# Kernel tuning notes

Measured on AMD Instinct MI355X. Metric: run time of the kernel, lower is better.

The kernel has to match this reference:

```python
import jax, jax.numpy as jnp
import numpy as np
from jax import lax

D_MODEL, D_STATE, D_CONV, EXPAND = 512, 16, 4, 2
D_INNER = EXPAND * D_MODEL          # 1024
DT_RANK = (D_MODEL + 15) // 16      # 32
BATCH, SEQ = 4, 1024


def setup_inputs() -> dict:
    key = jax.random.key(0)
    ks = jax.random.split(key, 8)
    s = 0.02
    x = jax.random.normal(ks[0], (BATCH, SEQ, D_MODEL), jnp.float32)
    in_proj_w = jax.random.normal(ks[1], (2 * D_INNER, D_MODEL), jnp.float32) * s
    conv_w = jax.random.normal(ks[2], (D_INNER, 1, D_CONV), jnp.float32) * s  # depthwise
    conv_b = jnp.zeros((D_INNER,), jnp.float32)
    x_proj_w = jax.random.normal(ks[3], (DT_RANK + 2 * D_STATE, D_INNER), jnp.float32) * s
    dt_proj_w = jax.random.normal(ks[4], (D_INNER, DT_RANK), jnp.float32) * s
    dt_proj_b = jax.random.normal(ks[5], (D_INNER,), jnp.float32) * 0.1
    # Mamba S4D-real init: A = -[1..d_state] per channel, stored as log
    A_log = jnp.log(jnp.tile(jnp.arange(1, D_STATE + 1, dtype=jnp.float32)[None, :], (D_INNER, 1)))
    D = jnp.ones((D_INNER,), jnp.float32)
    out_proj_w = jax.random.normal(ks[6], (D_MODEL, D_INNER), jnp.float32) * s
    ln_w = jnp.ones((D_MODEL,), jnp.float32)
    ln_b = jnp.zeros((D_MODEL,), jnp.float32)
    return dict(x=x, in_proj_w=in_proj_w, conv_w=conv_w, conv_b=conv_b,
                x_proj_w=x_proj_w, dt_proj_w=dt_proj_w, dt_proj_b=dt_proj_b,
                A_log=A_log, D=D, out_proj_w=out_proj_w, ln_w=ln_w, ln_b=ln_b)


def _selective_scan(u, delta, A, Bm, Cm, D):
    # u, delta: (B,L,Di); A: (Di,N); Bm, Cm: (B,L,N)
    dA = jnp.exp(delta[..., None] * A)                    # (B,L,Di,N)
    dBu = (delta * u)[..., None] * Bm[:, :, None, :]      # (B,L,Di,N)
    dA_t = jnp.moveaxis(dA, 1, 0)                         # (L,B,Di,N)
    dBu_t = jnp.moveaxis(dBu, 1, 0)
    C_t = jnp.moveaxis(Cm, 1, 0)                          # (L,B,N)

    def step(h, inp):
        dA_i, dBu_i, C_i = inp
        h = dA_i * h + dBu_i                              # (B,Di,N)
        y = jnp.einsum('bdn,bn->bd', h, C_i)
        return h, y

    h0 = jnp.zeros((u.shape[0], A.shape[0], A.shape[1]), u.dtype)
    _, ys = lax.scan(step, h0, (dA_t, dBu_t, C_t))        # ys: (L,B,Di)
    return jnp.moveaxis(ys, 0, 1) + u * D                 # (B,L,Di)


def reference(x, in_proj_w, conv_w, conv_b, x_proj_w, dt_proj_w, dt_proj_b,
              A_log, D, out_proj_w, ln_w, ln_b):
    # ---- Mamba SSM ----
    xz = jnp.einsum('bld,ed->ble', x, in_proj_w)          # (B,L,2*Di)
    xs, z = jnp.split(xz, 2, axis=-1)
    # causal depthwise conv over time
    xt = jnp.moveaxis(xs, 1, 2)                           # (B,Di,L)
    xt = lax.conv_general_dilated(xt, conv_w, window_strides=(1,),
                                  padding=[(D_CONV - 1, 0)],
                                  feature_group_count=D_INNER,
                                  dimension_numbers=('NCH', 'OIH', 'NCH'))
    xt = xt + conv_b[None, :, None]
    u = jax.nn.silu(jnp.moveaxis(xt, 1, 2))               # (B,L,Di)

    x_dbl = jnp.einsum('bld,ed->ble', u, x_proj_w)        # (B,L,dt_rank+2N)
    dt = x_dbl[..., :DT_RANK]
    Bm = x_dbl[..., DT_RANK:DT_RANK + D_STATE]
    Cm = x_dbl[..., DT_RANK + D_STATE:]
    delta = jax.nn.softplus(jnp.einsum('blr,dr->bld', dt, dt_proj_w) + dt_proj_b)
    A = -jnp.exp(A_log)                                   # (Di,N)

    y = _selective_scan(u, delta, A, Bm, Cm, D)
    y = y * jax.nn.silu(z)
    ssm_out = jnp.einsum('ble,de->bld', y, out_proj_w)    # (B,L,Dm)

    # ---- residual + LayerNorm ----
    r = x + ssm_out
    mu = jnp.mean(r, axis=-1, keepdims=True)
    var = jnp.mean(jnp.square(r - mu), axis=-1, keepdims=True)
    return (r - mu) / jnp.sqrt(var + 1e-5) * ln_w + ln_b
```

## Files before the change

kernel.cpp:

```cpp
#include <hip/hip_runtime.h>
#include <hip/hip_bf16.h>
#include <math.h>

#define B_   4
#define L_   1024
#define DM   512
#define DI   1024
#define NS   16
#define XDC  64
#define BL   4096
#define G_   16
#define SEG  64
#define KS   4

typedef short bfrag __attribute__((ext_vector_type(8)));
typedef float ffrag __attribute__((ext_vector_type(4)));

__device__ __forceinline__ ushort f2bf(float v) {
    __hip_bfloat16 h = __float2bfloat16(v);
    return *(ushort*)&h;
}

__global__ __launch_bounds__(256) void cast_bf16(const float* __restrict__ in,
        ushort* __restrict__ out, int n4)
{
    int i = blockIdx.x * 256 + threadIdx.x;
    if (i >= n4) return;
    float4 v = ((const float4*)in)[i];
    ushort4 o;
    o.x = f2bf(v.x); o.y = f2bf(v.y); o.z = f2bf(v.z); o.w = f2bf(v.w);
    ((ushort4*)out)[i] = o;
}

template<int EPI>
__global__ __launch_bounds__(256) void gemm_mfma(const ushort* __restrict__ A,
        const ushort* __restrict__ B, float* __restrict__ C,
        int K, int ldc, const float* __restrict__ resid,
        const float* __restrict__ bias)
{
    __shared__ ushort As[128][40];
    __shared__ ushort Bs[128][40];
    const int tid = threadIdx.x;
    const int lane = tid & 63, wave = tid >> 6;
    const int wm = (wave & 1) * 64, wn = (wave >> 1) * 64;
    const int l15 = lane & 15, quad = lane >> 4;
    const int m0 = blockIdx.y * 128, n0 = blockIdx.x * 128;

    ffrag acc[4][4] = {};

    for (int k0 = 0; k0 < K; k0 += 32) {
        #pragma unroll
        for (int i = 0; i < 2; i++) {
            int chunk = tid + i * 256;
            int row = chunk >> 2, kk8 = (chunk & 3) * 8;
            *(uint4*)&As[row][kk8] = *(const uint4*)&A[(size_t)(m0 + row) * K + k0 + kk8];
            *(uint4*)&Bs[row][kk8] = *(const uint4*)&B[(size_t)(n0 + row) * K + k0 + kk8];
        }
        __syncthreads();
        bfrag af[4], bfv[4];
        #pragma unroll
        for (int i = 0; i < 4; i++) {
            af[i]  = *(const bfrag*)&As[wm + i * 16 + l15][quad * 8];
            bfv[i] = *(const bfrag*)&Bs[wn + i * 16 + l15][quad * 8];
        }
        #pragma unroll
        for (int i = 0; i < 4; i++)
            #pragma unroll
            for (int j = 0; j < 4; j++)
                acc[i][j] = __builtin_amdgcn_mfma_f32_16x16x32_bf16(af[i], bfv[j], acc[i][j], 0, 0, 0);
        __syncthreads();
    }

    #pragma unroll
    for (int i = 0; i < 4; i++) {
        #pragma unroll
        for (int j = 0; j < 4; j++) {
            int n = n0 + wn + j * 16 + l15;
            #pragma unroll
            for (int r = 0; r < 4; r++) {
                int m = m0 + wm + i * 16 + quad * 4 + r;
                float v = acc[i][j][r];
                if (EPI == 2) v += resid[(size_t)m * ldc + n];
                if (EPI == 3) {
                    v += bias[m];
                    v = (v > 20.f) ? v : log1pf(__expf(v));
                }
                C[(size_t)m * ldc + n] = v;
            }
        }
    }
}

__global__ __launch_bounds__(256) void gemm3_splitk(const float* __restrict__ uT,
        const float* __restrict__ xw, float* __restrict__ part)
{
    __shared__ float As[16][33];
    __shared__ float Ws[16][68];
    const int tid = threadIdx.x;
    const int tx = tid & 15, ty = tid >> 4;
    const int ks = blockIdx.x, m0 = blockIdx.y * 32;
    const int kbase = ks * (DI / KS);
    float acc[2][4] = {};

    for (int k0 = 0; k0 < DI / KS; k0 += 16) {
        if (tid < 128) {
            int k = tid >> 3, m4 = (tid & 7) * 4;
            const float4 v = *(const float4*)&uT[(size_t)(kbase + k0 + k) * BL + m0 + m4];
            As[k][m4 + 0] = v.x; As[k][m4 + 1] = v.y;
            As[k][m4 + 2] = v.z; As[k][m4 + 3] = v.w;
        }
        {
            int r = tid >> 2, c4 = (tid & 3) * 4;
            const float4 v = *(const float4*)&xw[(size_t)r * DI + kbase + k0 + c4];
            Ws[c4 + 0][r] = v.x; Ws[c4 + 1][r] = v.y;
            Ws[c4 + 2][r] = v.z; Ws[c4 + 3][r] = v.w;
        }
        __syncthreads();
        #pragma unroll
        for (int kk = 0; kk < 16; kk++) {
            float a[2], b[4];
            a[0] = As[kk][ty * 2 + 0];
            a[1] = As[kk][ty * 2 + 1];
            #pragma unroll
            for (int j = 0; j < 4; j++) b[j] = Ws[kk][tx * 4 + j];
            #pragma unroll
            for (int i = 0; i < 2; i++)
                #pragma unroll
                for (int j = 0; j < 4; j++)
                    acc[i][j] = fmaf(a[i], b[j], acc[i][j]);
        }
        __syncthreads();
    }

    float* pp = part + (size_t)ks * BL * XDC;
    #pragma unroll
    for (int i = 0; i < 2; i++) {
        int m = m0 + ty * 2 + i;
        *(float4*)&pp[(size_t)m * XDC + tx * 4] =
            make_float4(acc[i][0], acc[i][1], acc[i][2], acc[i][3]);
    }
}

__global__ __launch_bounds__(256) void gemm3_reduce(const float* __restrict__ part,
        float* __restrict__ xdbl, ushort* __restrict__ dtB)
{
    int i = blockIdx.x * 256 + threadIdx.x;
    const float4* p0 = (const float4*)part;
    float4 a = p0[i];
    #pragma unroll
    for (int s = 1; s < KS; s++) {
        float4 b = p0[i + (size_t)s * BL * XDC / 4];
        a.x += b.x; a.y += b.y; a.z += b.z; a.w += b.w;
    }
    ((float4*)xdbl)[i] = a;
    int c4 = i & 15;
    if (c4 < 8) {
        int m = i >> 4;
        ushort4 o;
        o.x = f2bf(a.x); o.y = f2bf(a.y); o.z = f2bf(a.z); o.w = f2bf(a.w);
        ((ushort4*)dtB)[m * 8 + c4] = o;
    }
}

__global__ __launch_bounds__(256) void conv_silu(const float* __restrict__ xzT,
        const float* __restrict__ cw, const float* __restrict__ cb,
        float* __restrict__ uT)
{
    int i = blockIdx.x * 256 + threadIdx.x;
    int d  = i >> 10;
    int q  = i & 1023;
    int bl = q * 4;
    int l  = bl & (L_ - 1);
    const float* row = xzT + (size_t)d * BL;
    float4 cur = *(const float4*)&row[bl];
    float4 prev = make_float4(0.f, 0.f, 0.f, 0.f);
    if (l != 0) prev = *(const float4*)&row[bl - 4];
    float v[7] = { prev.y, prev.z, prev.w, cur.x, cur.y, cur.z, cur.w };
    float w0 = cw[d * 4 + 0], w1 = cw[d * 4 + 1], w2 = cw[d * 4 + 2], w3 = cw[d * 4 + 3];
    float bias = cb[d];
    float4 o;
    o.x = bias + w0 * v[0] + w1 * v[1] + w2 * v[2] + w3 * v[3];
    o.y = bias + w0 * v[1] + w1 * v[2] + w2 * v[3] + w3 * v[4];
    o.z = bias + w0 * v[2] + w1 * v[3] + w2 * v[4] + w3 * v[5];
    o.w = bias + w0 * v[3] + w1 * v[4] + w2 * v[5] + w3 * v[6];
    o.x = o.x / (1.f + __expf(-o.x));
    o.y = o.y / (1.f + __expf(-o.y));
    o.z = o.z / (1.f + __expf(-o.z));
    o.w = o.w / (1.f + __expf(-o.w));
    *(float4*)&uT[(size_t)d * BL + bl] = o;
}

__global__ __launch_bounds__(256) void scan_fused(const float* __restrict__ deltaT,
        const float* __restrict__ uT, const float* __restrict__ xdbl,
        const float* __restrict__ xzT, const float* __restrict__ A_log,
        const float* __restrict__ Dp, float* __restrict__ yT)
{
    __shared__ float hend_s[G_][NS + 1];
    __shared__ float h0_s[G_][NS + 1];
    __shared__ float sdv_s[G_];

    const int tid = threadIdx.x;
    const int n = tid & 15;
    const int seg = tid >> 4;
    const int bd = blockIdx.x;
    const int d = bd & (DI - 1);
    const int b = bd >> 10;

    const float Acoef = -__expf(A_log[d * NS + n]);
    const float Dd = Dp[d];

    const size_t base_t = (size_t)d * BL + b * L_ + seg * SEG;
    const size_t base_z = (size_t)(DI + d) * BL + b * L_ + seg * SEG;
    const size_t base_x = (size_t)b * L_ * XDC + (size_t)seg * SEG * XDC;

    float h = 0.f, sdv = 0.f;
    for (int l0 = 0; l0 < SEG; l0 += 16) {
        float dv[16], uv[16], Bv[16];
        {
            const float4* dp = (const float4*)(deltaT + base_t + l0);
            const float4* up = (const float4*)(uT + base_t + l0);
            #pragma unroll
            for (int i = 0; i < 4; i++) {
                *(float4*)&dv[i * 4] = dp[i];
                *(float4*)&uv[i * 4] = up[i];
            }
        }
        {
            const float* xp = xdbl + base_x + (size_t)l0 * XDC + 32 + n;
            #pragma unroll
            for (int j = 0; j < 16; j++) Bv[j] = xp[j * XDC];
        }
        #pragma unroll
        for (int j = 0; j < 16; j++) {
            sdv += dv[j];
            Bv[j] *= dv[j] * uv[j];
            dv[j] = __expf(dv[j] * Acoef);
        }
        #pragma unroll
        for (int j = 0; j < 16; j++)
            h = fmaf(dv[j], h, Bv[j]);
    }
    hend_s[seg][n] = h;
    if (n == 0) sdv_s[seg] = sdv;
    __syncthreads();

    if (seg == 0) {
        float H = 0.f;
        #pragma unroll
        for (int s = 0; s < G_; s++) {
            h0_s[s][n] = H;
            H = hend_s[s][n] + __expf(Acoef * sdv_s[s]) * H;
        }
    }
    __syncthreads();

    h = h0_s[seg][n];
    for (int l0 = 0; l0 < SEG; l0 += 16) {
        float ug = uT [base_t + l0 + n];
        float zg = xzT[base_z + l0 + n];

        float dv[16], uv[16];
        {
            const float4* dp = (const float4*)(deltaT + base_t + l0);
            const float4* up = (const float4*)(uT + base_t + l0);
            #pragma unroll
            for (int i = 0; i < 4; i++) {
                *(float4*)&dv[i * 4] = dp[i];
                *(float4*)&uv[i * 4] = up[i];
            }
        }
        float Bv[16], Cv[16];
        {
            const float* xp = xdbl + base_x + (size_t)l0 * XDC + 32 + n;
            #pragma unroll
            for (int j = 0; j < 16; j++) {
                Bv[j] = xp[j * XDC];
                Cv[j] = xp[j * XDC + 16];
            }
        }
        #pragma unroll
        for (int j = 0; j < 16; j++) {
            Bv[j] *= dv[j] * uv[j];
            dv[j] = __expf(dv[j] * Acoef);
        }
        float p[16];
        #pragma unroll
        for (int j = 0; j < 16; j++) {
            h = fmaf(dv[j], h, Bv[j]);
            p[j] = h * Cv[j];
        }

        float q8[8];
        #pragma unroll
        for (int k = 0; k < 8; k++) {
            float tt = (n & 8) ? p[k] : p[k + 8];
            float rr = __shfl_xor(tt, 8);
            q8[k] = ((n & 8) ? p[k + 8] : p[k]) + rr;
        }
        float q4[4];
        #pragma unroll
        for (int k = 0; k < 4; k++) {
            float tt = (n & 4) ? q8[k] : q8[k + 4];
            float rr = __shfl_xor(tt, 4);
            q4[k] = ((n & 4) ? q8[k + 4] : q8[k]) + rr;
        }
        float q2[2];
        #pragma unroll
        for (int k = 0; k < 2; k++) {
            float tt = (n & 2) ? q4[k] : q4[k + 2];
            float rr = __shfl_xor(tt, 2);
            q2[k] = ((n & 2) ? q4[k + 2] : q4[k]) + rr;
        }
        float tt = (n & 1) ? q2[0] : q2[1];
        float rr = __shfl_xor(tt, 1);
        float S = ((n & 1) ? q2[1] : q2[0]) + rr;

        float v = S + ug * Dd;
        v *= zg / (1.f + __expf(-zg));
        yT[base_t + l0 + n] = v;
    }
}

__global__ __launch_bounds__(256) void transpose_cast(const float* __restrict__ yT,
        ushort* __restrict__ yB)
{
    __shared__ float t[64][65];
    const int bl0 = blockIdx.x * 64, d0 = blockIdx.y * 64;
    const int tid = threadIdx.x;
    #pragma unroll
    for (int i = 0; i < 4; i++) {
        int chunk = tid + i * 256;
        int dr = chunk >> 4, c4 = (chunk & 15) * 4;
        const float4 v = *(const float4*)&yT[(size_t)(d0 + dr) * BL + bl0 + c4];
        t[dr][c4 + 0] = v.x; t[dr][c4 + 1] = v.y;
        t[dr][c4 + 2] = v.z; t[dr][c4 + 3] = v.w;
    }
    __syncthreads();
    #pragma unroll
    for (int i = 0; i < 4; i++) {
        int chunk = tid + i * 256;
        int br = chunk >> 4, dc4 = (chunk & 15) * 4;
        ushort4 o;
        o.x = f2bf(t[dc4 + 0][br]); o.y = f2bf(t[dc4 + 1][br]);
        o.z = f2bf(t[dc4 + 2][br]); o.w = f2bf(t[dc4 + 3][br]);
        *(ushort4*)&yB[(size_t)(bl0 + br) * DI + d0 + dc4] = o;
    }
}

__global__ __launch_bounds__(256) void ln_kernel(const float* __restrict__ r,
        const float* __restrict__ lnw, const float* __restrict__ lnb,
        float* __restrict__ out)
{
    int row = blockIdx.x;
    const float* rr = r + (size_t)row * DM;
    float v0 = rr[threadIdx.x], v1 = rr[threadIdx.x + 256];
    float s = v0 + v1, s2 = v0 * v0 + v1 * v1;
    #pragma unroll
    for (int off = 32; off > 0; off >>= 1) {
        s  += __shfl_down(s, off);
        s2 += __shfl_down(s2, off);
    }
    __shared__ float ls[4], ls2[4];
    __shared__ float mu_s, rstd_s;
    int wid = threadIdx.x >> 6, lane = threadIdx.x & 63;
    if (lane == 0) { ls[wid] = s; ls2[wid] = s2; }
    __syncthreads();
    if (threadIdx.x == 0) {
        float S = ls[0] + ls[1] + ls[2] + ls[3];
        float S2 = ls2[0] + ls2[1] + ls2[2] + ls2[3];
        float mu = S * (1.f / DM);
        float var = S2 * (1.f / DM) - mu * mu;
        mu_s = mu;
        rstd_s = rsqrtf(var + 1e-5f);
    }
    __syncthreads();
    float mu = mu_s, rstd = rstd_s;
    out[(size_t)row * DM + threadIdx.x] =
        (v0 - mu) * rstd * lnw[threadIdx.x] + lnb[threadIdx.x];
    out[(size_t)row * DM + threadIdx.x + 256] =
        (v1 - mu) * rstd * lnw[threadIdx.x + 256] + lnb[threadIdx.x + 256];
}

extern "C" void kernel_launch(void* const* d_in, const int* in_sizes, int n_in,
                              void* d_out, int out_size, void* d_ws, size_t ws_size,
                              hipStream_t stream)
{
    const float* x         = (const float*)d_in[0];
    const float* in_proj_w = (const float*)d_in[1];
    const float* conv_w    = (const float*)d_in[2];
    const float* conv_b    = (const float*)d_in[3];
    const float* x_proj_w  = (const float*)d_in[4];
    const float* dt_proj_w = (const float*)d_in[5];
    const float* dt_proj_b = (const float*)d_in[6];
    const float* A_log     = (const float*)d_in[7];
    const float* Dvec      = (const float*)d_in[8];
    const float* out_proj_w= (const float*)d_in[9];
    const float* ln_w      = (const float*)d_in[10];
    const float* ln_b      = (const float*)d_in[11];
    float* out = (float*)d_out;

    float* ws     = (float*)d_ws;
    float* xzT    = ws;
    float* uT     = xzT    + (size_t)2048 * BL;
    float* xdbl   = uT     + (size_t)DI * BL;
    float* deltaT = xdbl   + (size_t)BL * XDC;
    float* yT     = deltaT + (size_t)DI * BL;
    float* r      = yT     + (size_t)DI * BL;
    ushort* xB    = (ushort*)yT;
    float*  xdblp = yT;
    ushort* yB    = (ushort*)deltaT;
    ushort* wOutB = (ushort*)deltaT + (size_t)4 * 1024 * 1024;
    ushort* wInB  = (ushort*)deltaT + (size_t)9 * 1024 * 1024 / 2;
    ushort* dtB   = (ushort*)r;
    ushort* dtwB  = (ushort*)r + (size_t)BL * 32;

    dim3 blk(256);

    cast_bf16<<<(BL * DM / 4 + 255) / 256, blk, 0, stream>>>(x, xB, BL * DM / 4);
    cast_bf16<<<(2048 * DM / 4 + 255) / 256, blk, 0, stream>>>(in_proj_w, wInB, 2048 * DM / 4);
    cast_bf16<<<(DI * 32 / 4 + 255) / 256, blk, 0, stream>>>(dt_proj_w, dtwB, DI * 32 / 4);

    gemm_mfma<0><<<dim3(BL / 128, 2048 / 128), blk, 0, stream>>>(
        wInB, xB, xzT, DM, BL, nullptr, nullptr);

    conv_silu<<<(DI * BL / 4) / 256, blk, 0, stream>>>(xzT, conv_w, conv_b, uT);

    gemm3_splitk<<<dim3(KS, BL / 32), blk, 0, stream>>>(uT, x_proj_w, xdblp);
    gemm3_reduce<<<(BL * XDC / 4) / 256, blk, 0, stream>>>(xdblp, xdbl, dtB);

    gemm_mfma<3><<<dim3(BL / 128, DI / 128), blk, 0, stream>>>(
        dtwB, dtB, deltaT, 32, BL, nullptr, dt_proj_b);

    scan_fused<<<B_ * DI, blk, 0, stream>>>(
        deltaT, uT, xdbl, xzT, A_log, Dvec, yT);

    transpose_cast<<<dim3(BL / 64, DI / 64), blk, 0, stream>>>(yT, yB);
    cast_bf16<<<(DM * DI / 4 + 255) / 256, blk, 0, stream>>>(out_proj_w, wOutB, DM * DI / 4);

    gemm_mfma<2><<<dim3(DM / 128, BL / 128), blk, 0, stream>>>(
        yB, wOutB, r, DI, DM, x, nullptr);

    ln_kernel<<<BL, blk, 0, stream>>>(r, ln_w, ln_b, out);
}
```

Measured before the change: 267.3 us.

## Parallelize selective scan with block-wide Hillis-Steele prefix over 64 segments

The scan kernel now launches 1024 threads per (batch, channel) block, splitting the 1024-step sequence into 64 segments of 16. The segments are combined with a log-step Hillis-Steele scan in shared memory, replacing the two-pass, 16-segment serial scan that reloaded inputs. The x_proj output is also stored transposed (feature-major), so B and C load as contiguous float4 rows instead of strided scalars; the split-K GEMM and reduce kernels are reworked to match. The cost is six block-wide barriers, more exp and multiply work in the prefix combine, and lower occupancy per CU from the larger blocks.

Result: slower. 310.5 us (+16.2%).

```diff
diff --git a/kernel.cpp b/kernel.cpp
--- a/kernel.cpp
+++ b/kernel.cpp
@@ -9,8 +9,8 @@
 #define NS   16
 #define XDC  64
 #define BL   4096
-#define G_   16
-#define SEG  64
+#define G2   64
+#define SEG2 16
 #define KS   4
 
 typedef short bfrag __attribute__((ext_vector_type(8)));
@@ -97,10 +97,11 @@
     __shared__ float As[16][33];
     __shared__ float Ws[16][68];
     const int tid = threadIdx.x;
-    const int tx = tid & 15, ty = tid >> 4;
+    const int nn = tid & 63;
+    const int mg = tid >> 6;
     const int ks = blockIdx.x, m0 = blockIdx.y * 32;
     const int kbase = ks * (DI / KS);
-    float acc[2][4] = {};
+    float acc[8] = {};
 
     for (int k0 = 0; k0 < DI / KS; k0 += 16) {
         if (tid < 128) {
@@ -118,47 +119,40 @@
         __syncthreads();
         #pragma unroll
         for (int kk = 0; kk < 16; kk++) {
-            float a[2], b[4];
-            a[0] = As[kk][ty * 2 + 0];
-            a[1] = As[kk][ty * 2 + 1];
+            float w = Ws[kk][nn];
             #pragma unroll
-            for (int j = 0; j < 4; j++) b[j] = Ws[kk][tx * 4 + j];
-            #pragma unroll
-            for (int i = 0; i < 2; i++)
-                #pragma unroll
-                for (int j = 0; j < 4; j++)
-                    acc[i][j] = fmaf(a[i], b[j], acc[i][j]);
+            for (int i = 0; i < 8; i++)
+                acc[i] = fmaf(As[kk][mg * 8 + i], w, acc[i]);
         }
         __syncthreads();
     }
 
-    float* pp = part + (size_t)ks * BL * XDC;
-    #pragma unroll
-    for (int i = 0; i < 2; i++) {
-        int m = m0 + ty * 2 + i;
-        *(float4*)&pp[(size_t)m * XDC + tx * 4] =
-            make_float4(acc[i][0], acc[i][1], acc[i][2], acc[i][3]);
-    }
+    float* pp = part + (size_t)ks * 64 * BL + (size_t)nn * BL + m0 + mg * 8;
+    *(float4*)&pp[0] = make_float4(acc[0], acc[1], acc[2], acc[3]);
+    *(float4*)&pp[4] = make_float4(acc[4], acc[5], acc[6], acc[7]);
 }
 
 __global__ __launch_bounds__(256) void gemm3_reduce(const float* __restrict__ part,
-        float* __restrict__ xdbl, ushort* __restrict__ dtB)
+        float* __restrict__ xdblT, ushort* __restrict__ dtB)
 {
     int i = blockIdx.x * 256 + threadIdx.x;
+    int n  = i >> 10;
+    int m4 = (i & 1023) * 4;
     const float4* p0 = (const float4*)part;
-    float4 a = p0[i];
+    size_t idx = ((size_t)n * BL + m4) >> 2;
+    float4 a = p0[idx];
     #pragma unroll
     for (int s = 1; s < KS; s++) {
-        float4 b = p0[i + (size_t)s * BL * XDC / 4];
-        a.x += b.x; a.y += b.y; a.z += b.z; a.w += b.w;
-    }
-    ((float4*)xdbl)[i] = a;
-    int c4 = i & 15;
-    if (c4 < 8) {
-        int m = i >> 4;
-        ushort4 o;
-        o.x = f2bf(a.x); o.y = f2bf(a.y); o.z = f2bf(a.z); o.w = f2bf(a.w);
-        ((ushort4*)dtB)[m * 8 + c4] = o;
+        float4 b2 = p0[idx + (size_t)s * 64 * BL / 4];
+        a.x += b2.x; a.y += b2.y; a.z += b2.z; a.w += b2.w;
+    }
+    if (n >= 32) {
+        *(float4*)&xdblT[(size_t)n * BL + m4] = a;
+    } else {
+        dtB[(size_t)(m4 + 0) * 32 + n] = f2bf(a.x);
+        dtB[(size_t)(m4 + 1) * 32 + n] = f2bf(a.y);
+        dtB[(size_t)(m4 + 2) * 32 + n] = f2bf(a.z);
+        dtB[(size_t)(m4 + 3) * 32 + n] = f2bf(a.w);
     }
 }
 
@@ -190,14 +184,13 @@
     *(float4*)&uT[(size_t)d * BL + bl] = o;
 }
 
-__global__ __launch_bounds__(256) void scan_fused(const float* __restrict__ deltaT,
-        const float* __restrict__ uT, const float* __restrict__ xdbl,
+__global__ __launch_bounds__(1024) void scan_fused(const float* __restrict__ deltaT,
+        const float* __restrict__ uT, const float* __restrict__ xdblT,
         const float* __restrict__ xzT, const float* __restrict__ A_log,
         const float* __restrict__ Dp, float* __restrict__ yT)
 {
-    __shared__ float hend_s[G_][NS + 1];
-    __shared__ float h0_s[G_][NS + 1];
-    __shared__ float sdv_s[G_];
+    __shared__ float fac_s[2][G2][NS];
+    __shared__ float hh_s[2][G2][NS];
 
     const int tid = threadIdx.x;
     const int n = tid & 15;
@@ -209,116 +202,89 @@
     const float Acoef = -__expf(A_log[d * NS + n]);
     const float Dd = Dp[d];
 
-    const size_t base_t = (size_t)d * BL + b * L_ + seg * SEG;
-    const size_t base_z = (size_t)(DI + d) * BL + b * L_ + seg * SEG;
-    const size_t base_x = (size_t)b * L_ * XDC + (size_t)seg * SEG * XDC;
-
-    float h = 0.f, sdv = 0.f;
-    for (int l0 = 0; l0 < SEG; l0 += 16) {
-        float dv[16], uv[16], Bv[16];
-        {
-            const float4* dp = (const float4*)(deltaT + base_t + l0);
-            const float4* up = (const float4*)(uT + base_t + l0);
-            #pragma unroll
-            for (int i = 0; i < 4; i++) {
-                *(float4*)&dv[i * 4] = dp[i];
-                *(float4*)&uv[i * 4] = up[i];
-            }
-        }
-        {
-            const float* xp = xdbl + base_x + (size_t)l0 * XDC + 32 + n;
-            #pragma unroll
-            for (int j = 0; j < 16; j++) Bv[j] = xp[j * XDC];
-        }
-        #pragma unroll
-        for (int j = 0; j < 16; j++) {
-            sdv += dv[j];
-            Bv[j] *= dv[j] * uv[j];
-            dv[j] = __expf(dv[j] * Acoef);
-        }
-        #pragma unroll
-        for (int j = 0; j < 16; j++)
-            h = fmaf(dv[j], h, Bv[j]);
-    }
-    hend_s[seg][n] = h;
-    if (n == 0) sdv_s[seg] = sdv;
+    const size_t base_t = (size_t)d * BL + b * L_ + seg * SEG2;
+    const size_t base_z = (size_t)(DI + d) * BL + b * L_ + seg * SEG2;
+    const size_t col0   = (size_t)b * L_ + seg * SEG2;
+
+    float dv[16], uv[16], Bv[16];
+    {
+        const float4* dp = (const float4*)(deltaT + base_t);
+        const float4* up = (const float4*)(uT + base_t);
+        const float4* bp = (const float4*)(xdblT + (size_t)(32 + n) * BL + col0);
+        #pragma unroll
+        for (int i = 0; i < 4; i++) {
+            *(float4*)&dv[i * 4] = dp[i];
+            *(float4*)&uv[i * 4] = up[i];
+            *(float4*)&Bv[i * 4] = bp[i];
+        }
+    }
+
+    float a = 1.f, bb = 0.f;
+    #pragma unroll
+    for (int j = 0; j < 16; j++) {
+        Bv[j] *= dv[j] * uv[j];
+        dv[j] = __expf(dv[j] * Acoef);
+        a *= dv[j];
+        bb = fmaf(dv[j], bb, Bv[j]);
+    }
+
+    fac_s[0][seg][n] = a; hh_s[0][seg][n] = bb;
     __syncthreads();
-
-    if (seg == 0) {
-        float H = 0.f;
-        #pragma unroll
-        for (int s = 0; s < G_; s++) {
-            h0_s[s][n] = H;
-            H = hend_s[s][n] + __expf(Acoef * sdv_s[s]) * H;
-        }
-    }
-    __syncthreads();
-
-    h = h0_s[seg][n];
-    for (int l0 = 0; l0 < SEG; l0 += 16) {
-        float ug = uT [base_t + l0 + n];
-        float zg = xzT[base_z + l0 + n];
-
-        float dv[16], uv[16];
-        {
-            const float4* dp = (const float4*)(deltaT + base_t + l0);
-            const float4* up = (const float4*)(uT + base_t + l0);
-            #pragma unroll
-            for (int i = 0; i < 4; i++) {
-                *(float4*)&dv[i * 4] = dp[i];
-                *(float4*)&uv[i * 4] = up[i];
-            }
-        }
-        float Bv[16], Cv[16];
-        {
-            const float* xp = xdbl + base_x + (size_t)l0 * XDC + 32 + n;
-            #pragma unroll
-            for (int j = 0; j < 16; j++) {
-                Bv[j] = xp[j * XDC];
-                Cv[j] = xp[j * XDC + 16];
-            }
-        }
-        #pragma unroll
-        for (int j = 0; j < 16; j++) {
-            Bv[j] *= dv[j] * uv[j];
-            dv[j] = __expf(dv[j] * Acoef);
-        }
-        float p[16];
-        #pragma unroll
-        for (int j = 0; j < 16; j++) {
-            h = fmaf(dv[j], h, Bv[j]);
-            p[j] = h * Cv[j];
-        }
-
-        float q8[8];
-        #pragma unroll
-        for (int k = 0; k < 8; k++) {
-            float tt = (n & 8) ? p[k] : p[k + 8];
-            float rr = __shfl_xor(tt, 8);
-            q8[k] = ((n & 8) ? p[k + 8] : p[k]) + rr;
-        }
-        float q4[4];
-        #pragma unroll
-        for (int k = 0; k < 4; k++) {
-            float tt = (n & 4) ? q8[k] : q8[k + 4];
-            float rr = __shfl_xor(tt, 4);
-            q4[k] = ((n & 4) ? q8[k + 4] : q8[k]) + rr;
-        }
-        float q2[2];
-        #pragma unroll
-        for (int k = 0; k < 2; k++) {
-            float tt = (n & 2) ? q4[k] : q4[k + 2];
-            float rr = __shfl_xor(tt, 2);
-            q2[k] = ((n & 2) ? q4[k + 2] : q4[k]) + rr;
-        }
-        float tt = (n & 1) ? q2[0] : q2[1];
-        float rr = __shfl_xor(tt, 1);
-        float S = ((n & 1) ? q2[1] : q2[0]) + rr;
-
-        float v = S + ug * Dd;
-        v *= zg / (1.f + __expf(-zg));
-        yT[base_t + l0 + n] = v;
-    }
+    int pp = 0;
+    #pragma unroll
+    for (int off = 1; off < G2; off <<= 1) {
+        float a1 = 1.f, b1 = 0.f;
+        if (seg >= off) { a1 = fac_s[pp][seg - off][n]; b1 = hh_s[pp][seg - off][n]; }
+        bb = fmaf(a, b1, bb);
+        a  = a * a1;
+        fac_s[pp ^ 1][seg][n] = a; hh_s[pp ^ 1][seg][n] = bb;
+        pp ^= 1;
+        __syncthreads();
+    }
+    float h = (seg == 0) ? 0.f : hh_s[pp][seg - 1][n];
+
+    float Cv[16];
+    {
+        const float4* cp = (const float4*)(xdblT + (size_t)(48 + n) * BL + col0);
+        #pragma unroll
+        for (int i = 0; i < 4; i++) *(float4*)&Cv[i * 4] = cp[i];
+    }
+    #pragma unroll
+    for (int j = 0; j < 16; j++) {
+        h = fmaf(dv[j], h, Bv[j]);
+        Cv[j] *= h;
+    }
+
+    float q8[8];
+    #pragma unroll
+    for (int k = 0; k < 8; k++) {
+        float tt = (n & 8) ? Cv[k] : Cv[k + 8];
+        float rr = __shfl_xor(tt, 8);
+        q8[k] = ((n & 8) ? Cv[k + 8] : Cv[k]) + rr;
+    }
+    float q4[4];
+    #pragma unroll
+    for (int k = 0; k < 4; k++) {
+        float tt = (n & 4) ? q8[k] : q8[k + 4];
+        float rr = __shfl_xor(tt, 4);
+        q4[k] = ((n & 4) ? q8[k + 4] : q8[k]) + rr;
+    }
+    float q2[2];
+    #pragma unroll
+    for (int k = 0; k < 2; k++) {
+        float tt = (n & 2) ? q4[k] : q4[k + 2];
+        float rr = __shfl_xor(tt, 2);
+        q2[k] = ((n & 2) ? q4[k + 2] : q4[k]) + rr;
+    }
+    float tt = (n & 1) ? q2[0] : q2[1];
+    float rr = __shfl_xor(tt, 1);
+    float S = ((n & 1) ? q2[1] : q2[0]) + rr;
+
+    float ug = uT [base_t + n];
+    float zg = xzT[base_z + n];
+    float v = S + ug * Dd;
+    v *= zg / (1.f + __expf(-zg));
+    yT[base_t + n] = v;
 }
 
 __global__ __launch_bounds__(256) void transpose_cast(const float* __restrict__ yT,
@@ -402,8 +368,8 @@
     float* ws     = (float*)d_ws;
     float* xzT    = ws;
     float* uT     = xzT    + (size_t)2048 * BL;
-    float* xdbl   = uT     + (size_t)DI * BL;
-    float* deltaT = xdbl   + (size_t)BL * XDC;
+    float* xdblT  = uT     + (size_t)DI * BL;
+    float* deltaT = xdblT  + (size_t)XDC * BL;
     float* yT     = deltaT + (size_t)DI * BL;
     float* r      = yT     + (size_t)DI * BL;
     ushort* xB    = (ushort*)yT;
@@ -426,13 +392,13 @@
     conv_silu<<<(DI * BL / 4) / 256, blk, 0, stream>>>(xzT, conv_w, conv_b, uT);
 
     gemm3_splitk<<<dim3(KS, BL / 32), blk, 0, stream>>>(uT, x_proj_w, xdblp);
-    gemm3_reduce<<<(BL * XDC / 4) / 256, blk, 0, stream>>>(xdblp, xdbl, dtB);
+    gemm3_reduce<<<(64 * BL / 4) / 256, blk, 0, stream>>>(xdblp, xdblT, dtB);
 
     gemm_mfma<3><<<dim3(BL / 128, DI / 128), blk, 0, stream>>>(
         dtwB, dtB, deltaT, 32, BL, nullptr, dt_proj_b);
 
-    scan_fused<<<B_ * DI, blk, 0, stream>>>(
-        deltaT, uT, xdbl, xzT, A_log, Dvec, yT);
+    scan_fused<<<B_ * DI, dim3(1024), 0, stream>>>(
+        deltaT, uT, xdblT, xzT, A_log, Dvec, yT);
 
     transpose_cast<<<dim3(BL / 64, DI / 64), blk, 0, stream>>>(yT, yB);
     cast_bf16<<<(DM * DI / 4 + 255) / 256, blk, 0, stream>>>(out_proj_w, wOutB, DM * DI / 4);
```

## Restructure selective scan as one wave per channel with lane-level prefix scan

Applied to the files above, without the earlier changes.

The scan kernel is reorganized so each 64-lane wave handles one (batch, channel) pair. Each lane owns 16 timesteps and all 16 state entries. Segment carries are combined with a warp-shuffle Kogge-Stone scan instead of shared memory, block barriers and a serial combine step. The C·h reduction becomes a per-lane FMA chain instead of cross-lane butterfly shuffles. The cost is heavier register pressure from the 16-wide state arrays and 32 shuffles per scan step.

Measured after the change: 337.0 us. +26.1%, slower.

```diff
diff --git a/kernel.cpp b/kernel.cpp
--- a/kernel.cpp
+++ b/kernel.cpp
@@ -9,8 +9,6 @@
 #define NS   16
 #define XDC  64
 #define BL   4096
-#define G_   16
-#define SEG  64
 #define KS   4
 
 typedef short bfrag __attribute__((ext_vector_type(8)));
@@ -195,129 +193,118 @@
         const float* __restrict__ xzT, const float* __restrict__ A_log,
         const float* __restrict__ Dp, float* __restrict__ yT)
 {
-    __shared__ float hend_s[G_][NS + 1];
-    __shared__ float h0_s[G_][NS + 1];
-    __shared__ float sdv_s[G_];
-
     const int tid = threadIdx.x;
-    const int n = tid & 15;
-    const int seg = tid >> 4;
-    const int bd = blockIdx.x;
+    const int lane = tid & 63;
+    const int w = tid >> 6;
+    const int bd = blockIdx.x * 4 + w;
     const int d = bd & (DI - 1);
     const int b = bd >> 10;
 
-    const float Acoef = -__expf(A_log[d * NS + n]);
+    const size_t base_t = (size_t)d * BL + b * L_ + lane * 16;
+    const size_t base_z = (size_t)(DI + d) * BL + b * L_ + lane * 16;
+    const float* xrow = xdbl + ((size_t)b * L_ + lane * 16) * XDC + 32;
+
+    float Acoef[16];
+    {
+        const float4* ap = (const float4*)(A_log + d * NS);
+        #pragma unroll
+        for (int i = 0; i < 4; i++) {
+            float4 v = ap[i];
+            Acoef[i * 4 + 0] = -__expf(v.x); Acoef[i * 4 + 1] = -__expf(v.y);
+            Acoef[i * 4 + 2] = -__expf(v.z); Acoef[i * 4 + 3] = -__expf(v.w);
+        }
+    }
+
+    float dv[16], uv[16];
+    {
+        const float4* dp = (const float4*)(deltaT + base_t);
+        const float4* up = (const float4*)(uT + base_t);
+        #pragma unroll
+        for (int i = 0; i < 4; i++) {
+            *(float4*)&dv[i * 4] = dp[i];
+            *(float4*)&uv[i * 4] = up[i];
+        }
+    }
+
+    float bb[16];
+    #pragma unroll
+    for (int n = 0; n < 16; n++) bb[n] = 0.f;
+    float sa = 0.f;
+    #pragma unroll
+    for (int j = 0; j < 16; j++) {
+        float Bv[16];
+        const float4* bp = (const float4*)(xrow + (size_t)j * XDC);
+        #pragma unroll
+        for (int i = 0; i < 4; i++) *(float4*)&Bv[i * 4] = bp[i];
+        float dl = dv[j], du = dl * uv[j];
+        sa += dl;
+        #pragma unroll
+        for (int n = 0; n < 16; n++) {
+            float t = __expf(dl * Acoef[n]);
+            bb[n] = fmaf(t, bb[n], du * Bv[n]);
+        }
+    }
+    float a[16];
+    #pragma unroll
+    for (int n = 0; n < 16; n++) a[n] = __expf(sa * Acoef[n]);
+
+    #pragma unroll
+    for (int off = 1; off < 64; off <<= 1) {
+        float pa[16], pb[16];
+        #pragma unroll
+        for (int n = 0; n < 16; n++) {
+            pa[n] = __shfl_up(a[n], off);
+            pb[n] = __shfl_up(bb[n], off);
+        }
+        if (lane >= off) {
+            #pragma unroll
+            for (int n = 0; n < 16; n++) {
+                bb[n] = fmaf(a[n], pb[n], bb[n]);
+                a[n] *= pa[n];
+            }
+        }
+    }
+
+    float h[16];
+    #pragma unroll
+    for (int n = 0; n < 16; n++) {
+        float pb = __shfl_up(bb[n], 1);
+        h[n] = (lane == 0) ? 0.f : pb;
+    }
+
+    float zg[16];
+    {
+        const float4* zp = (const float4*)(xzT + base_z);
+        #pragma unroll
+        for (int i = 0; i < 4; i++) *(float4*)&zg[i * 4] = zp[i];
+    }
     const float Dd = Dp[d];
-
-    const size_t base_t = (size_t)d * BL + b * L_ + seg * SEG;
-    const size_t base_z = (size_t)(DI + d) * BL + b * L_ + seg * SEG;
-    const size_t base_x = (size_t)b * L_ * XDC + (size_t)seg * SEG * XDC;
-
-    float h = 0.f, sdv = 0.f;
-    for (int l0 = 0; l0 < SEG; l0 += 16) {
-        float dv[16], uv[16], Bv[16];
-        {
-            const float4* dp = (const float4*)(deltaT + base_t + l0);
-            const float4* up = (const float4*)(uT + base_t + l0);
-            #pragma unroll
-            for (int i = 0; i < 4; i++) {
-                *(float4*)&dv[i * 4] = dp[i];
-                *(float4*)&uv[i * 4] = up[i];
-            }
-        }
-        {
-            const float* xp = xdbl + base_x + (size_t)l0 * XDC + 32 + n;
-            #pragma unroll
-            for (int j = 0; j < 16; j++) Bv[j] = xp[j * XDC];
-        }
-        #pragma unroll
-        for (int j = 0; j < 16; j++) {
-            sdv += dv[j];
-            Bv[j] *= dv[j] * uv[j];
-            dv[j] = __expf(dv[j] * Acoef);
-        }
-        #pragma unroll
-        for (int j = 0; j < 16; j++)
-            h = fmaf(dv[j], h, Bv[j]);
-    }
-    hend_s[seg][n] = h;
-    if (n == 0) sdv_s[seg] = sdv;
-    __syncthreads();
-
-    if (seg == 0) {
-        float H = 0.f;
-        #pragma unroll
-        for (int s = 0; s < G_; s++) {
-            h0_s[s][n] = H;
-            H = hend_s[s][n] + __expf(Acoef * sdv_s[s]) * H;
-        }
-    }
-    __syncthreads();
-
-    h = h0_s[seg][n];
-    for (int l0 = 0; l0 < SEG; l0 += 16) {
-        float ug = uT [base_t + l0 + n];
-        float zg = xzT[base_z + l0 + n];
-
-        float dv[16], uv[16];
-        {
-            const float4* dp = (const float4*)(deltaT + base_t + l0);
-            const float4* up = (const float4*)(uT + base_t + l0);
-            #pragma unroll
-            for (int i = 0; i < 4; i++) {
-                *(float4*)&dv[i * 4] = dp[i];
-                *(float4*)&uv[i * 4] = up[i];
-            }
-        }
+    #pragma unroll
+    for (int j = 0; j < 16; j++) {
         float Bv[16], Cv[16];
-        {
-            const float* xp = xdbl + base_x + (size_t)l0 * XDC + 32 + n;
-            #pragma unroll
-            for (int j = 0; j < 16; j++) {
-                Bv[j] = xp[j * XDC];
-                Cv[j] = xp[j * XDC + 16];
-            }
-        }
-        #pragma unroll
-        for (int j = 0; j < 16; j++) {
-            Bv[j] *= dv[j] * uv[j];
-            dv[j] = __expf(dv[j] * Acoef);
-        }
-        float p[16];
-        #pragma unroll
-        for (int j = 0; j < 16; j++) {
-            h = fmaf(dv[j], h, Bv[j]);
-            p[j] = h * Cv[j];
-        }
-
-        float q8[8];
-        #pragma unroll
-        for (int k = 0; k < 8; k++) {
-            float tt = (n & 8) ? p[k] : p[k + 8];
-            float rr = __shfl_xor(tt, 8);
-            q8[k] = ((n & 8) ? p[k + 8] : p[k]) + rr;
-        }
-        float q4[4];
-        #pragma unroll
-        for (int k = 0; k < 4; k++) {
-            float tt = (n & 4) ? q8[k] : q8[k + 4];
-            float rr = __shfl_xor(tt, 4);
-            q4[k] = ((n & 4) ? q8[k + 4] : q8[k]) + rr;
-        }
-        float q2[2];
-        #pragma unroll
-        for (int k = 0; k < 2; k++) {
-            float tt = (n & 2) ? q4[k] : q4[k + 2];
-            float rr = __shfl_xor(tt, 2);
-            q2[k] = ((n & 2) ? q4[k + 2] : q4[k]) + rr;
-        }
-        float tt = (n & 1) ? q2[0] : q2[1];
-        float rr = __shfl_xor(tt, 1);
-        float S = ((n & 1) ? q2[1] : q2[0]) + rr;
-
-        float v = S + ug * Dd;
-        v *= zg / (1.f + __expf(-zg));
-        yT[base_t + l0 + n] = v;
+        const float4* bp = (const float4*)(xrow + (size_t)j * XDC);
+        const float4* cp = (const float4*)(xrow + (size_t)j * XDC + 16);
+        #pragma unroll
+        for (int i = 0; i < 4; i++) {
+            *(float4*)&Bv[i * 4] = bp[i];
+            *(float4*)&Cv[i * 4] = cp[i];
+        }
+        float dl = dv[j], du = dl * uv[j];
+        float s = 0.f;
+        #pragma unroll
+        for (int n = 0; n < 16; n++) {
+            float t = __expf(dl * Acoef[n]);
+            h[n] = fmaf(t, h[n], du * Bv[n]);
+            s = fmaf(h[n], Cv[n], s);
+        }
+        float val = s + uv[j] * Dd;
+        float z = zg[j];
+        zg[j] = val * (z / (1.f + __expf(-z)));
+    }
+    {
+        float4* yp = (float4*)(yT + base_t);
+        #pragma unroll
+        for (int i = 0; i < 4; i++) yp[i] = *(float4*)&zg[i * 4];
     }
 }
 
@@ -431,7 +418,7 @@
     gemm_mfma<3><<<dim3(BL / 128, DI / 128), blk, 0, stream>>>(
         dtwB, dtB, deltaT, 32, BL, nullptr, dt_proj_b);
 
-    scan_fused<<<B_ * DI, blk, 0, stream>>>(
+    scan_fused<<<B_ * DI / 4, blk, 0, stream>>>(
         deltaT, uT, xdbl, xzT, A_log, Dvec, yT);
 
     transpose_cast<<<dim3(BL / 64, DI / 64), blk, 0, stream>>>(yT, yB);
```
